# Optimization experiments

Measured on AMD Instinct MI355X. Metric: run time of the kernel, lower is better.

## Reference

```python
import jax, jax.numpy as jnp
import numpy as np

EMBED_DIM = 2048
NUM_HEADS = 16
HEAD_DIM = EMBED_DIM // NUM_HEADS
BATCH, SEQ = 4, 4096


def setup_inputs() -> dict:
    key = jax.random.key(0)
    k1, k2, k3, k4 = jax.random.split(key, 4)
    scale = 1.0 / np.sqrt(EMBED_DIM)
    x = jax.random.normal(k1, (BATCH, SEQ, EMBED_DIM), dtype=jnp.float32)
    W_qkv = jax.random.normal(k2, (EMBED_DIM, 3 * EMBED_DIM), dtype=jnp.float32) * scale
    W_out = jax.random.normal(k3, (EMBED_DIM, EMBED_DIM), dtype=jnp.float32) * scale
    b_out = jax.random.normal(k4, (EMBED_DIM,), dtype=jnp.float32) * 0.01
    return {"x": x, "W_qkv": W_qkv, "W_out": W_out, "b_out": b_out}


def reference(x, W_qkv, W_out, b_out):
    b, s, _ = x.shape
    # qkv: (b, s, 3, h, d)
    qkv = (x @ W_qkv).reshape(b, s, 3, NUM_HEADS, HEAD_DIM)
    q, k, v = qkv[:, :, 0], qkv[:, :, 1], qkv[:, :, 2]
    # NOTE: faithful to source — scores mix HEADS per token: (b, s, h, h)
    scores = jnp.einsum('bshd,bsHd->bshH', q, k) / jnp.sqrt(jnp.float32(HEAD_DIM))
    w = jax.nn.softmax(scores, axis=-1)
    attn = jnp.einsum('bshH,bsHd->bshd', w, v).reshape(b, s, EMBED_DIM)
    return attn @ W_out + b_out
```

## Files before the change

### kernel.cpp

```cpp
#include <hip/hip_runtime.h>
#include <hip/hip_bf16.h>
#include <cstdint>


#define TOKENS 16384
#define EMB    2048
#define NQKV   6144

typedef __bf16 bf16x8_t __attribute__((ext_vector_type(8)));
typedef float  f32x4_t  __attribute__((ext_vector_type(4)));
typedef unsigned short ushort8_t __attribute__((ext_vector_type(8)));

#define GLOAD16(gsrc, ldst)                                                    \
  __builtin_amdgcn_global_load_lds(                                            \
      (const __attribute__((address_space(1))) void*)(uintptr_t)(gsrc),        \
      (__attribute__((address_space(3))) void*)(uint32_t)(uintptr_t)(ldst),    \
      16, 0, 0)

static __device__ __forceinline__ unsigned short f32_to_bf16_bits(float f) {
  union { float f; uint32_t u; } x; x.f = f;
  uint32_t u = x.u;
  u += 0x7fffu + ((u >> 16) & 1u);
  return (unsigned short)(u >> 16);
}

static __device__ __forceinline__ unsigned int pack_bf16(float lo, float hi) {
  return ((unsigned int)f32_to_bf16_bits(hi) << 16) | (unsigned int)f32_to_bf16_bits(lo);
}

__global__ __launch_bounds__(256) void prep(
    const float4* __restrict__ x4, ushort4* __restrict__ xb4,
    const float* __restrict__ Wqkv, unsigned short* __restrict__ wqkvT,
    const float* __restrict__ Wout, unsigned short* __restrict__ woutT) {
  const int b = blockIdx.x;
  const int t = threadIdx.x;
  if (b < 2048) {
    const int n4 = 33554432 / 4;
    const int stride = 2048 * 256;
    for (int i = b * 256 + t; i < n4; i += stride) {
      float4 v = x4[i];
      ushort4 o;
      o.x = f32_to_bf16_bits(v.x);
      o.y = f32_to_bf16_bits(v.y);
      o.z = f32_to_bf16_bits(v.z);
      o.w = f32_to_bf16_bits(v.w);
      xb4[i] = o;
    }
    return;
  }
  __shared__ float tile[32][33];
  const float* in;
  unsigned short* out;
  int R, C, bxt, byt;
  if (b < 14336) {
    const int bb = b - 2048;
    in = Wqkv; out = wqkvT; R = 2048; C = 6144;
    bxt = bb % 192; byt = bb / 192;
  } else {
    const int bb = b - 14336;
    in = Wout; out = woutT; R = 2048; C = 2048;
    bxt = bb % 64; byt = bb / 64;
  }
  const int bx = bxt * 32;
  const int by = byt * 32;
  const int tx = t & 31;
  const int ty = t >> 5;
#pragma unroll
  for (int j = 0; j < 32; j += 8)
    tile[ty + j][tx] = in[(size_t)(by + ty + j) * C + bx + tx];
  __syncthreads();
#pragma unroll
  for (int j = 0; j < 32; j += 8)
    out[(size_t)(bx + ty + j) * R + by + tx] = f32_to_bf16_bits(tile[tx][ty + j]);
}

template <bool OUT_BF16>
__global__ __launch_bounds__(512, 1) void gemm_bt(
    const unsigned short* __restrict__ A,
    const unsigned short* __restrict__ BT,
    unsigned short* __restrict__ Cb,
    float* __restrict__ Cf,
    const float* __restrict__ bias,
    int M, int N) {
  constexpr int K = 2048;
  constexpr int BK = 64;
  constexpr int NKT = K / BK;
  __shared__ __align__(16) char lds[131072];

  const int nbx = N / 256;
  const int nwg = gridDim.x;
  const int bid = blockIdx.x;
  const int swzb = (bid & 7) * (nwg >> 3) + (bid >> 3);
  const int by = swzb / nbx;
  const int bx = swzb % nbx;

  const int t    = threadIdx.x;
  const int lane = t & 63;
  const int wid  = t >> 6;
  const int wr   = wid >> 2;
  const int wc   = wid & 3;
  const int lr   = lane & 15;
  const int g    = lane >> 4;
  const bool g0  = (wr == 0);

  const unsigned short* aSrc = A  + (size_t)by * 256 * K;
  const unsigned short* bSrc = BT + (size_t)bx * 256 * K;

  int aoff[2], boff[2];
#pragma unroll
  for (int i = 0; i < 2; ++i) {
    const int p   = (i * 512 + t) * 16;
    const int lo  = p ^ (((p >> 7) & 7) << 4);
    const int rih = lo >> 7;
    const int kbe = (lo & 127) >> 1;
    aoff[i] = (((rih >> 6) << 7) + (rih & 63)) * K + kbe;
    boff[i] = (((rih >> 5) << 6) + (rih & 31)) * K + kbe;
  }
  const int ldst = wid << 10;

  auto stageA = [&](int h, int k0, char* bufA) {
#pragma unroll
    for (int i = 0; i < 2; ++i)
      GLOAD16(aSrc + aoff[i] + h * (64 * K) + k0, bufA + h * 16384 + i * 8192 + ldst);
  };
  auto stageB = [&](int h, int k0, char* bufB) {
#pragma unroll
    for (int i = 0; i < 2; ++i)
      GLOAD16(bSrc + boff[i] + h * (32 * K) + k0, bufB + h * 16384 + i * 8192 + ldst);
  };

  const int sw   = (lr & 7) << 4;
  const int col0 = (g * 16) ^ sw;
  const int col1 = (64 + g * 16) ^ sw;
  const int aRow = (wr * 64 + lr) * 128;
  const int bRow = (wc * 32 + lr) * 128;

  f32x4_t acc[8][4] = {};
  bf16x8_t av[4][2];
  bf16x8_t bv0[2][2], bv1[2][2];

#define LDA_INTO(dst, bufA_, q)                                                \
  {                                                                            \
    const char* _b = (bufA_) + (q) * 16384 + aRow;                             \
    _Pragma("unroll") for (int m2 = 0; m2 < 4; ++m2) {                         \
      dst[m2][0] = *(const bf16x8_t*)(_b + m2 * 2048 + col0);                  \
      dst[m2][1] = *(const bf16x8_t*)(_b + m2 * 2048 + col1);                  \
    }                                                                          \
  }
#define LDB_INTO(dst, bufB_, pair)                                             \
  {                                                                            \
    _Pragma("unroll") for (int e = 0; e < 2; ++e) {                            \
      const int nf = (pair) * 2 + e;                                           \
      const char* _b = (bufB_) + (nf >> 1) * 16384 + (nf & 1) * 2048 + bRow;   \
      dst[e][0] = *(const bf16x8_t*)(_b + col0);                               \
      dst[e][1] = *(const bf16x8_t*)(_b + col1);                               \
    }                                                                          \
  }
#define MFMAQ(AV, BV, Q, PAIR)                                                 \
  _Pragma("unroll") for (int m2 = 0; m2 < 4; ++m2)                             \
  _Pragma("unroll") for (int e = 0; e < 2; ++e)                                \
  _Pragma("unroll") for (int ks = 0; ks < 2; ++ks)                             \
    acc[(Q) * 4 + m2][(PAIR) * 2 + e] = __builtin_amdgcn_mfma_f32_16x16x32_bf16( \
        AV[m2][ks], BV[e][ks], acc[(Q) * 4 + m2][(PAIR) * 2 + e], 0, 0, 0);

#define SBR __builtin_amdgcn_sched_barrier(0)
#define BARR __builtin_amdgcn_s_barrier()
#define LGKM0 asm volatile("s_waitcnt lgkmcnt(0)" ::: "memory"); SBR;
#define P1_ __builtin_amdgcn_s_setprio(1);
#define P0_ __builtin_amdgcn_s_setprio(0); SBR;

#define MQ0 { LGKM0; P1_; MFMAQ(av, bv0, 0, 0); MFMAQ(av, bv1, 0, 1); P0_; }
#define MQ1 { LGKM0; P1_; MFMAQ(av, bv0, 1, 0); MFMAQ(av, bv1, 1, 1); P0_; }

#define BODY(KT, SA1, SB2, VMN, MP)                                            \
  {                                                                            \
    char* cA = lds + ((KT) & 1) * 65536;                                       \
    char* cB = cA + 32768;                                                     \
    char* nA = lds + (((KT) + 1) & 1) * 65536;                                 \
    const int k1 = ((KT) + 1) * BK, k2 = ((KT) + 2) * BK;                      \
    if (g0) { LDA_INTO(av, cA, 0); LDB_INTO(bv0, cB, 0); LDB_INTO(bv1, cB, 1); } \
    SBR;                                                                       \
    if (SA1) { stageA(0, k1, nA); } SBR;                                       \
    if (!g0 && (MP)) MQ1;                                                      \
    SBR; BARR;                                                                 \
    if (!g0) { LDA_INTO(av, cA, 0); LDB_INTO(bv0, cB, 0); LDB_INTO(bv1, cB, 1); } \
    SBR;                                                                       \
    if (SA1) { stageA(1, k1, nA); } SBR;                                       \
    if (g0) MQ0;                                                               \
    SBR; BARR;                                                                 \
    if (g0) { LDA_INTO(av, cA, 1); } SBR;                                      \
    if (!g0) MQ0;                                                              \
    SBR; BARR;                                                                 \
    if (!g0) { LDA_INTO(av, cA, 1); } SBR;                                     \
    if (SB2) { stageB(0, k2, cB); stageB(1, k2, cB); } SBR;                    \
    asm volatile("s_waitcnt vmcnt(" #VMN ")" ::: "memory"); SBR;               \
    if (g0) MQ1;                                                               \
    SBR; BARR;                                                                 \
  }

  {
    char* b0A = lds;
    char* b0B = lds + 32768;
    char* b1B = lds + 65536 + 32768;
    stageB(0, 0, b0B); stageB(1, 0, b0B);
    stageA(0, 0, b0A);
    stageA(1, 0, b0A);
    stageB(0, BK, b1B); stageB(1, BK, b1B);
    asm volatile("s_waitcnt vmcnt(4)" ::: "memory");
    BARR;
  }

  BODY(0, 1, 1, 4, 0);
  for (int kt = 1; kt < NKT - 2; ++kt) {
    BODY(kt, 1, 1, 4, 1);
  }
  BODY(NKT - 2, 1, 0, 0, 1);
  BODY(NKT - 1, 0, 0, 0, 1);
  if (!g0) MQ1;

  const int rbase = by * 256 + wr * 128 + g * 4;
  const int cbase = bx * 256 + wc * 64 + lr;
#pragma unroll
  for (int m = 0; m < 8; ++m) {
#pragma unroll
    for (int nf = 0; nf < 4; ++nf) {
      const int col = cbase + nf * 16;
#pragma unroll
      for (int j = 0; j < 4; ++j) {
        const size_t off = (size_t)(rbase + (m >> 2) * 64 + (m & 3) * 16 + j) * N + col;
        if constexpr (OUT_BF16) {
          Cb[off] = f32_to_bf16_bits(acc[m][nf][j]);
        } else {
          Cf[off] = acc[m][nf][j] + bias[col];
        }
      }
    }
  }
#undef LDA_INTO
#undef LDB_INTO
#undef MFMAQ
#undef SBR
#undef BARR
#undef LGKM0
#undef P1_
#undef P0_
#undef MQ0
#undef MQ1
#undef BODY
}

__global__ __launch_bounds__(256) void attn_mfma(
    const unsigned short* __restrict__ qkv,
    unsigned short* __restrict__ attn) {
  __shared__ __align__(16) unsigned short sV[4][2048];

  const int t  = threadIdx.x;
  const int w  = t >> 6;
  const int l  = t & 63;
  const int lr = l & 15;
  const int g  = l >> 4;
  const size_t tok = (size_t)blockIdx.x * 4 + w;
  const unsigned short* base = qkv + tok * NQKV;

  {
    const uint4* vg = (const uint4*)(base + 4096);
    uint4* vl = (uint4*)&sV[w][0];
#pragma unroll
    for (int i = 0; i < 4; ++i) {
      const int idx = i * 64 + l;
      uint4 v = vg[idx];
      if (idx & 128) {
        uint4 o; o.x = v.y; o.y = v.x; o.z = v.w; o.w = v.z;
        vl[idx] = o;
      } else {
        vl[idx] = v;
      }
    }
  }

  f32x4_t s = {};
#pragma unroll
  for (int ch = 0; ch < 4; ++ch) {
    bf16x8_t ka = *(const bf16x8_t*)(base + 2048 + lr * 128 + ch * 32 + g * 8);
    bf16x8_t qb = *(const bf16x8_t*)(base +        lr * 128 + ch * 32 + g * 8);
    s = __builtin_amdgcn_mfma_f32_16x16x32_bf16(ka, qb, s, 0, 0, 0);
  }

  float p0 = s[0] * 0.08838834764831843f;
  float p1 = s[1] * 0.08838834764831843f;
  float p2 = s[2] * 0.08838834764831843f;
  float p3 = s[3] * 0.08838834764831843f;
  float mx = fmaxf(fmaxf(p0, p1), fmaxf(p2, p3));
  mx = fmaxf(mx, __shfl_xor(mx, 16));
  mx = fmaxf(mx, __shfl_xor(mx, 32));
  p0 = __expf(p0 - mx);
  p1 = __expf(p1 - mx);
  p2 = __expf(p2 - mx);
  p3 = __expf(p3 - mx);
  float sum = p0 + p1 + p2 + p3;
  sum += __shfl_xor(sum, 16);
  sum += __shfl_xor(sum, 32);
  const float inv = 1.0f / sum;

  const unsigned int u01 = pack_bf16(p0, p1);
  const unsigned int u23 = pack_bf16(p2, p3);
  const int gs = (g & 1) * 2;
  const int m1 = (gs << 4) | lr;
  const int m2 = m1 + 16;
  union { uint4 u; bf16x8_t b; } pB;
  pB.u.x = __shfl(u01, m1);
  pB.u.y = __shfl(u23, m1);
  pB.u.z = __shfl(u01, m2);
  pB.u.w = __shfl(u23, m2);
  if (g >= 2) { pB.u.x = 0; pB.u.y = 0; pB.u.z = 0; pB.u.w = 0; }

  const char* vbase = (const char*)&sV[w][0];
  const int dbyte = (lr * 2) ^ (g < 2 ? (g << 2) : 0);
#pragma unroll
  for (int ch = 0; ch < 8; ++ch) {
    union { ushort8_t u; bf16x8_t b; } va;
    if (g < 2) {
#pragma unroll
      for (int j = 0; j < 8; ++j) {
        const int H = g * 8 + j;
        va.u[j] = *(const unsigned short*)(vbase + H * 256 + ch * 32 + dbyte);
      }
    } else {
      va.u = (ushort8_t){0, 0, 0, 0, 0, 0, 0, 0};
    }
    f32x4_t z = {};
    f32x4_t o = __builtin_amdgcn_mfma_f32_16x16x32_bf16(va.b, pB.b, z, 0, 0, 0);
    uint2 st;
    st.x = pack_bf16(o[0] * inv, o[1] * inv);
    st.y = pack_bf16(o[2] * inv, o[3] * inv);
    *(uint2*)(attn + tok * EMB + lr * 128 + ch * 16 + g * 4) = st;
  }
}

extern "C" void kernel_launch(void* const* d_in, const int* in_sizes, int n_in,
                              void* d_out, int out_size, void* d_ws, size_t ws_size,
                              hipStream_t stream) {
  const float* x    = (const float*)d_in[0];
  const float* Wqkv = (const float*)d_in[1];
  const float* Wout = (const float*)d_in[2];
  const float* bout = (const float*)d_in[3];
  float* out = (float*)d_out;

  unsigned short* xb    = (unsigned short*)d_ws;
  unsigned short* wqkvT = xb    + (size_t)33554432;
  unsigned short* woutT = wqkvT + (size_t)12582912;
  unsigned short* qkv   = woutT + (size_t)4194304;
  unsigned short* attn  = qkv   + (size_t)100663296;

  prep<<<18432, 256, 0, stream>>>((const float4*)x, (ushort4*)xb,
                                  Wqkv, wqkvT, Wout, woutT);
  gemm_bt<true><<<(16384 / 256) * (6144 / 256), 512, 0, stream>>>(
      xb, wqkvT, qkv, nullptr, nullptr, 16384, 6144);
  attn_mfma<<<TOKENS / 4, 256, 0, stream>>>(qkv, attn);
  gemm_bt<false><<<(16384 / 256) * (2048 / 256), 512, 0, stream>>>(
      attn, woutT, nullptr, out, bout, 16384, 2048);
}
```

Before: 583.1 us.

## Shrink GEMM tile to 128x128 with 4 waves and two blocks per CU

The bf16 GEMM changes from a 256x256 tile with 8 waves and 128KB of LDS to a 128x128 tile with 4 waves, 64KB of LDS and launch bounds allowing two blocks per CU. The ping-pong schedule, where two wave groups alternated MFMA and LDS-read phases, is replaced by a simpler per-k-step pipeline: load all fragments, then two MFMA halves with global-to-LDS staging placed between them. The aim is to gain latency hiding from co-resident blocks and more workgroups. In exchange, arithmetic intensity per byte of global traffic drops because the tile is smaller, and the hand-tuned intra-block wave overlap is lost.

```diff
diff --git a/kernel.cpp b/kernel.cpp
--- a/kernel.cpp
+++ b/kernel.cpp
@@ -75,7 +75,7 @@
 }
 
 template <bool OUT_BF16>
-__global__ __launch_bounds__(512, 1) void gemm_bt(
+__global__ __launch_bounds__(256, 2) void gemm_bt(
     const unsigned short* __restrict__ A,
     const unsigned short* __restrict__ BT,
     unsigned short* __restrict__ Cb,
@@ -85,9 +85,9 @@
   constexpr int K = 2048;
   constexpr int BK = 64;
   constexpr int NKT = K / BK;
-  __shared__ __align__(16) char lds[131072];
-
-  const int nbx = N / 256;
+  __shared__ __align__(16) char lds[65536];
+
+  const int nbx = N / 128;
   const int nwg = gridDim.x;
   const int bid = blockIdx.x;
   const int swzb = (bid & 7) * (nwg >> 3) + (bid >> 3);
@@ -97,155 +97,134 @@
   const int t    = threadIdx.x;
   const int lane = t & 63;
   const int wid  = t >> 6;
-  const int wr   = wid >> 2;
-  const int wc   = wid & 3;
+  const int wr   = wid >> 1;
+  const int wc   = wid & 1;
   const int lr   = lane & 15;
   const int g    = lane >> 4;
-  const bool g0  = (wr == 0);
-
-  const unsigned short* aSrc = A  + (size_t)by * 256 * K;
-  const unsigned short* bSrc = BT + (size_t)bx * 256 * K;
-
-  int aoff[2], boff[2];
+
+  const unsigned short* aSrc = A  + (size_t)by * 128 * K;
+  const unsigned short* bSrc = BT + (size_t)bx * 128 * K;
+
+  int ahoff[2], bfoff[4];
 #pragma unroll
   for (int i = 0; i < 2; ++i) {
-    const int p   = (i * 512 + t) * 16;
+    const int p   = (i * 256 + t) * 16;
     const int lo  = p ^ (((p >> 7) & 7) << 4);
-    const int rih = lo >> 7;
-    const int kbe = (lo & 127) >> 1;
-    aoff[i] = (((rih >> 6) << 7) + (rih & 63)) * K + kbe;
-    boff[i] = (((rih >> 5) << 6) + (rih & 31)) * K + kbe;
+    ahoff[i] = (lo >> 7) * K + ((lo & 127) >> 1);
+  }
+#pragma unroll
+  for (int i = 0; i < 4; ++i) {
+    const int p   = (i * 256 + t) * 16;
+    const int lo  = p ^ (((p >> 7) & 7) << 4);
+    bfoff[i] = (lo >> 7) * K + ((lo & 127) >> 1);
   }
   const int ldst = wid << 10;
 
   auto stageA = [&](int h, int k0, char* bufA) {
 #pragma unroll
     for (int i = 0; i < 2; ++i)
-      GLOAD16(aSrc + aoff[i] + h * (64 * K) + k0, bufA + h * 16384 + i * 8192 + ldst);
+      GLOAD16(aSrc + ahoff[i] + h * (64 * K) + k0, bufA + h * 8192 + i * 4096 + ldst);
   };
-  auto stageB = [&](int h, int k0, char* bufB) {
-#pragma unroll
-    for (int i = 0; i < 2; ++i)
-      GLOAD16(bSrc + boff[i] + h * (32 * K) + k0, bufB + h * 16384 + i * 8192 + ldst);
+  auto stageB = [&](int k0, char* bufB) {
+#pragma unroll
+    for (int i = 0; i < 4; ++i)
+      GLOAD16(bSrc + bfoff[i] + k0, bufB + i * 4096 + ldst);
   };
 
   const int sw   = (lr & 7) << 4;
   const int col0 = (g * 16) ^ sw;
   const int col1 = (64 + g * 16) ^ sw;
   const int aRow = (wr * 64 + lr) * 128;
-  const int bRow = (wc * 32 + lr) * 128;
-
-  f32x4_t acc[8][4] = {};
+  const int bRow = (wc * 64 + lr) * 128;
+
+  f32x4_t acc[4][4] = {};
   bf16x8_t av[4][2];
-  bf16x8_t bv0[2][2], bv1[2][2];
-
-#define LDA_INTO(dst, bufA_, q)                                                \
+  bf16x8_t bv[4][2];
+
+#define LDA_ALL(cA_)                                                           \
+  _Pragma("unroll") for (int mf = 0; mf < 4; ++mf) {                           \
+    av[mf][0] = *(const bf16x8_t*)((cA_) + aRow + mf * 2048 + col0);           \
+    av[mf][1] = *(const bf16x8_t*)((cA_) + aRow + mf * 2048 + col1);           \
+  }
+#define LDB_ALL(cB_)                                                           \
+  _Pragma("unroll") for (int nf = 0; nf < 4; ++nf) {                           \
+    bv[nf][0] = *(const bf16x8_t*)((cB_) + bRow + nf * 2048 + col0);           \
+    bv[nf][1] = *(const bf16x8_t*)((cB_) + bRow + nf * 2048 + col1);           \
+  }
+#define MFMA_NF(NF0)                                                           \
+  _Pragma("unroll") for (int mf = 0; mf < 4; ++mf)                             \
+  _Pragma("unroll") for (int nf = (NF0); nf < (NF0) + 2; ++nf)                 \
+  _Pragma("unroll") for (int ks = 0; ks < 2; ++ks)                             \
+    acc[mf][nf] = __builtin_amdgcn_mfma_f32_16x16x32_bf16(                     \
+        av[mf][ks], bv[nf][ks], acc[mf][nf], 0, 0, 0);
+
+#define SBR __builtin_amdgcn_sched_barrier(0)
+
+#define BODY(KT, S1, S2, VMN)                                                  \
   {                                                                            \
-    const char* _b = (bufA_) + (q) * 16384 + aRow;                             \
-    _Pragma("unroll") for (int m2 = 0; m2 < 4; ++m2) {                         \
-      dst[m2][0] = *(const bf16x8_t*)(_b + m2 * 2048 + col0);                  \
-      dst[m2][1] = *(const bf16x8_t*)(_b + m2 * 2048 + col1);                  \
-    }                                                                          \
-  }
-#define LDB_INTO(dst, bufB_, pair)                                             \
-  {                                                                            \
-    _Pragma("unroll") for (int e = 0; e < 2; ++e) {                            \
-      const int nf = (pair) * 2 + e;                                           \
-      const char* _b = (bufB_) + (nf >> 1) * 16384 + (nf & 1) * 2048 + bRow;   \
-      dst[e][0] = *(const bf16x8_t*)(_b + col0);                               \
-      dst[e][1] = *(const bf16x8_t*)(_b + col1);                               \
-    }                                                                          \
-  }
-#define MFMAQ(AV, BV, Q, PAIR)                                                 \
-  _Pragma("unroll") for (int m2 = 0; m2 < 4; ++m2)                             \
-  _Pragma("unroll") for (int e = 0; e < 2; ++e)                                \
-  _Pragma("unroll") for (int ks = 0; ks < 2; ++ks)                             \
-    acc[(Q) * 4 + m2][(PAIR) * 2 + e] = __builtin_amdgcn_mfma_f32_16x16x32_bf16( \
-        AV[m2][ks], BV[e][ks], acc[(Q) * 4 + m2][(PAIR) * 2 + e], 0, 0, 0);
-
-#define SBR __builtin_amdgcn_sched_barrier(0)
-#define BARR __builtin_amdgcn_s_barrier()
-#define LGKM0 asm volatile("s_waitcnt lgkmcnt(0)" ::: "memory"); SBR;
-#define P1_ __builtin_amdgcn_s_setprio(1);
-#define P0_ __builtin_amdgcn_s_setprio(0); SBR;
-
-#define MQ0 { LGKM0; P1_; MFMAQ(av, bv0, 0, 0); MFMAQ(av, bv1, 0, 1); P0_; }
-#define MQ1 { LGKM0; P1_; MFMAQ(av, bv0, 1, 0); MFMAQ(av, bv1, 1, 1); P0_; }
-
-#define BODY(KT, SA1, SB2, VMN, MP)                                            \
-  {                                                                            \
-    char* cA = lds + ((KT) & 1) * 65536;                                       \
-    char* cB = cA + 32768;                                                     \
-    char* nA = lds + (((KT) + 1) & 1) * 65536;                                 \
+    char* cA = lds + ((KT) & 1) * 32768;                                       \
+    char* cB = cA + 16384;                                                     \
+    char* nA = lds + (((KT) + 1) & 1) * 32768;                                 \
     const int k1 = ((KT) + 1) * BK, k2 = ((KT) + 2) * BK;                      \
-    if (g0) { LDA_INTO(av, cA, 0); LDB_INTO(bv0, cB, 0); LDB_INTO(bv1, cB, 1); } \
-    SBR;                                                                       \
-    if (SA1) { stageA(0, k1, nA); } SBR;                                       \
-    if (!g0 && (MP)) MQ1;                                                      \
-    SBR; BARR;                                                                 \
-    if (!g0) { LDA_INTO(av, cA, 0); LDB_INTO(bv0, cB, 0); LDB_INTO(bv1, cB, 1); } \
-    SBR;                                                                       \
-    if (SA1) { stageA(1, k1, nA); } SBR;                                       \
-    if (g0) MQ0;                                                               \
-    SBR; BARR;                                                                 \
-    if (g0) { LDA_INTO(av, cA, 1); } SBR;                                      \
-    if (!g0) MQ0;                                                              \
-    SBR; BARR;                                                                 \
-    if (!g0) { LDA_INTO(av, cA, 1); } SBR;                                     \
-    if (SB2) { stageB(0, k2, cB); stageB(1, k2, cB); } SBR;                    \
+           \
+    LDA_ALL(cA);                                                               \
+    LDB_ALL(cB); SBR;                                                          \
+    if (S1) { stageA(1, k1, nA); } SBR;                                        \
+    asm volatile("s_waitcnt lgkmcnt(0)" ::: "memory"); SBR;                    \
+    __builtin_amdgcn_s_setprio(1);                                             \
+    MFMA_NF(0);                                                                \
+    __builtin_amdgcn_s_setprio(0); SBR;                                        \
+    __builtin_amdgcn_s_barrier();                                              \
+        \
+    if (S2) { stageB(k2, cB); stageA(0, k2, cA); } SBR;                        \
+    __builtin_amdgcn_s_setprio(1);                                             \
+    MFMA_NF(2);                                                                \
+    __builtin_amdgcn_s_setprio(0); SBR;                                        \
     asm volatile("s_waitcnt vmcnt(" #VMN ")" ::: "memory"); SBR;               \
-    if (g0) MQ1;                                                               \
-    SBR; BARR;                                                                 \
+    __builtin_amdgcn_s_barrier();                                              \
   }
 
   {
     char* b0A = lds;
-    char* b0B = lds + 32768;
-    char* b1B = lds + 65536 + 32768;
-    stageB(0, 0, b0B); stageB(1, 0, b0B);
-    stageA(0, 0, b0A);
-    stageA(1, 0, b0A);
-    stageB(0, BK, b1B); stageB(1, BK, b1B);
-    asm volatile("s_waitcnt vmcnt(4)" ::: "memory");
-    BARR;
-  }
-
-  BODY(0, 1, 1, 4, 0);
-  for (int kt = 1; kt < NKT - 2; ++kt) {
-    BODY(kt, 1, 1, 4, 1);
-  }
-  BODY(NKT - 2, 1, 0, 0, 1);
-  BODY(NKT - 1, 0, 0, 0, 1);
-  if (!g0) MQ1;
-
-  const int rbase = by * 256 + wr * 128 + g * 4;
-  const int cbase = bx * 256 + wc * 64 + lr;
-#pragma unroll
-  for (int m = 0; m < 8; ++m) {
+    char* b0B = lds + 16384;
+    char* b1A = lds + 32768;
+    char* b1B = b1A + 16384;
+    stageA(0, 0, b0A); stageA(1, 0, b0A);
+    stageB(0, b0B);
+    stageB(BK, b1B);
+    stageA(0, BK, b1A);
+    asm volatile("s_waitcnt vmcnt(6)" ::: "memory");
+    __builtin_amdgcn_s_barrier();
+  }
+
+  for (int kt = 0; kt < NKT - 2; ++kt) {
+    BODY(kt, 1, 1, 6);
+  }
+  BODY(NKT - 2, 1, 0, 0);
+  BODY(NKT - 1, 0, 0, 0);
+
+  const int rbase = by * 128 + wr * 64 + g * 4;
+  const int cbase = bx * 128 + wc * 64 + lr;
+#pragma unroll
+  for (int mf = 0; mf < 4; ++mf) {
 #pragma unroll
     for (int nf = 0; nf < 4; ++nf) {
       const int col = cbase + nf * 16;
 #pragma unroll
       for (int j = 0; j < 4; ++j) {
-        const size_t off = (size_t)(rbase + (m >> 2) * 64 + (m & 3) * 16 + j) * N + col;
+        const size_t off = (size_t)(rbase + mf * 16 + j) * N + col;
         if constexpr (OUT_BF16) {
-          Cb[off] = f32_to_bf16_bits(acc[m][nf][j]);
+          Cb[off] = f32_to_bf16_bits(acc[mf][nf][j]);
         } else {
-          Cf[off] = acc[m][nf][j] + bias[col];
+          Cf[off] = acc[mf][nf][j] + bias[col];
         }
       }
     }
   }
-#undef LDA_INTO
-#undef LDB_INTO
-#undef MFMAQ
+#undef LDA_ALL
+#undef LDB_ALL
+#undef MFMA_NF
 #undef SBR
-#undef BARR
-#undef LGKM0
-#undef P1_
-#undef P0_
-#undef MQ0
-#undef MQ1
 #undef BODY
 }
 
@@ -354,9 +333,9 @@
 
   prep<<<18432, 256, 0, stream>>>((const float4*)x, (ushort4*)xb,
                                   Wqkv, wqkvT, Wout, woutT);
-  gemm_bt<true><<<(16384 / 256) * (6144 / 256), 512, 0, stream>>>(
+  gemm_bt<true><<<(16384 / 128) * (6144 / 128), 256, 0, stream>>>(
       xb, wqkvT, qkv, nullptr, nullptr, 16384, 6144);
   attn_mfma<<<TOKENS / 4, 256, 0, stream>>>(qkv, attn);
-  gemm_bt<false><<<(16384 / 256) * (2048 / 256), 512, 0, stream>>>(
+  gemm_bt<false><<<(16384 / 128) * (2048 / 128), 256, 0, stream>>>(
       attn, woutT, nullptr, out, bout, 16384, 2048);
 }
```

Measured after the change: 749.4 us. +28.5%, slower.
